# Kernel tuning notes

Hardware: AMD Instinct MI355X
Metric: run time of the kernel (lower is better)

The kernel has to match this reference:

```python
import jax, jax.numpy as jnp
import numpy as np

N_NODES = 50000
N_EDGES = 1600000
IN_CH = 128
OUT_CH = 128
MAX_NORM = 1.0


def setup_inputs() -> dict:
    key = jax.random.key(0)
    k1, k2, k3, k4 = jax.random.split(key, 4)
    x = jax.random.normal(k1, (N_NODES, IN_CH), dtype=jnp.float32)
    edge_index = jax.random.randint(k2, (2, N_EDGES), 0, N_NODES, dtype=jnp.int64)
    # GCNConv lin: weight [out, in] (kaiming-ish init), bias [out] zeros-ish
    W = jax.random.normal(k3, (OUT_CH, IN_CH), dtype=jnp.float32) * (1.0 / np.sqrt(IN_CH))
    b = jax.random.normal(k4, (OUT_CH,), dtype=jnp.float32) * 0.01
    return {"x": x, "edge_index": edge_index, "W": W, "b": b}


def _renorm_cols(W, max_norm):
    # torch.renorm(W, p=2, dim=1, maxnorm): each slice along dim 1 (column of [out,in])
    # is rescaled so its L2 norm <= max_norm.
    norms = jnp.sqrt(jnp.sum(W * W, axis=0, keepdims=True))  # [1, in]
    scale = jnp.where(norms > max_norm, max_norm / norms, 1.0)
    return W * scale


def reference(x, edge_index, W, b):
    N = x.shape[0]
    Wn = _renorm_cols(W, MAX_NORM)
    # Linear transform first (as PyG GCNConv does): h = x @ W^T
    h = jnp.einsum('ni,oi->no', x, Wn)  # [N, out]

    # Add self loops
    row = jnp.concatenate([edge_index[0], jnp.arange(N, dtype=edge_index.dtype)])
    col = jnp.concatenate([edge_index[1], jnp.arange(N, dtype=edge_index.dtype)])

    # Symmetric normalization: deg over destination (col), edge weights = 1
    ones = jnp.ones(row.shape[0], dtype=h.dtype)
    deg = jax.ops.segment_sum(ones, col, num_segments=N)
    deg_inv_sqrt = jnp.where(deg > 0, jax.lax.rsqrt(deg), 0.0)
    norm = deg_inv_sqrt[row] * deg_inv_sqrt[col]  # [E+N]

    # Gather source features, scale, scatter-add to destinations
    msgs = h[row] * norm[:, None]  # [E+N, out]
    out = jax.ops.segment_sum(msgs, col, num_segments=N)
    return out + b
```

## Files before the change

kernel.cpp:

```cpp
#include <hip/hip_runtime.h>

#define N_NODES 50000
#define N_EDGES 1600000
#define CH 128
#define NB 196
#define CHUNK_E 2048
#define NCHUNK 782
#define CAP 12288

#define WS_CURSOR  0
#define WS_ROWPTR  1024
#define WS_DINV    201728
#define WS_SCL     401728
#define WS_SRC     601728
#define WS_Q8      7001728
#define WS_BINS    13401728

typedef __bf16 bf16x8 __attribute__((ext_vector_type(8)));
typedef float f32x4 __attribute__((ext_vector_type(4)));

__device__ __forceinline__ unsigned int pack_bf16(float a, float b) {
    unsigned int ua = __builtin_bit_cast(unsigned int, a);
    unsigned int ub = __builtin_bit_cast(unsigned int, b);
    ua = (ua + 0x7FFFu + ((ua >> 16) & 1u)) >> 16;
    ub = (ub + 0x7FFFu + ((ub >> 16) & 1u)) >> 16;
    return ua | (ub << 16);
}

__global__ __launch_bounds__(256) void k_binA(const int* __restrict__ eidx,
                                              int* __restrict__ cursor,
                                              unsigned int* __restrict__ bins) {
    __shared__ int lc[256];
    __shared__ int lbase[256];
    __shared__ unsigned int stash[CHUNK_E];
    __shared__ int s_st;
    int t = threadIdx.x, c = blockIdx.x;
    lc[t] = 0;
    if (t < 64) {
        int v = eidx[2 * t + 1];
        unsigned long long m = __ballot(v == 0);
        if (t == 0) s_st = (m == ~0ull) ? 2 : 1;
    }
    __syncthreads();
    int st = s_st;
    long base = (long)c * CHUNK_E;
    #pragma unroll
    for (int i = 0; i < CHUNK_E / 256; ++i) {
        long e = base + i * 256 + t;
        unsigned int u = 0xFFFFFFFFu;
        if (e < N_EDGES) {
            int row = eidx[(size_t)st * (size_t)e];
            int col = eidx[(size_t)st * (size_t)(N_EDGES + e)];
            u = (unsigned int)row | ((unsigned int)col << 16);
            atomicAdd(&lc[col >> 8], 1);
        }
        stash[i * 256 + t] = u;
    }
    __syncthreads();
    if (t < NB && lc[t] > 0) lbase[t] = atomicAdd(&cursor[t], lc[t]);
    __syncthreads();
    #pragma unroll
    for (int i = 0; i < CHUNK_E / 256; ++i) {
        unsigned int u = stash[i * 256 + t];
        if (u != 0xFFFFFFFFu) {
            int bb = u >> 24;
            int pos = atomicAdd(&lbase[bb], 1);
            bins[(size_t)bb * CAP + pos] = (u & 0xFFFFu) | (((u >> 16) & 0xFFu) << 16);
        }
    }
}

__global__ __launch_bounds__(256) void k_sort(const unsigned int* __restrict__ bins,
                                              const int* __restrict__ cursor,
                                              int* __restrict__ rowptr,
                                              float* __restrict__ dinv,
                                              int* __restrict__ src) {
    __shared__ int shA[256], shB[256], shC[256];
    __shared__ int s_g0, s_sz;
    int t = threadIdx.x, b = blockIdx.x;
    int v = (t < NB) ? cursor[t] : 0;
    shC[t] = v;
    __syncthreads();
    for (int off = 1; off < 256; off <<= 1) {
        int u = (t >= off) ? shC[t - off] : 0;
        __syncthreads();
        shC[t] += u;
        __syncthreads();
    }
    if (t == b) { s_g0 = shC[t] - v; s_sz = v; }
    __syncthreads();
    int g0 = s_g0, sz = s_sz;
    const unsigned int* reg = bins + (size_t)b * CAP;
    shA[t] = 0;
    __syncthreads();
    for (int i = t; i < sz; i += 256) {
        unsigned int p = reg[i];
        atomicAdd(&shA[(p >> 16) & 255], 1);
    }
    __syncthreads();
    int d = shA[t];
    shC[t] = d;
    __syncthreads();
    for (int off = 1; off < 256; off <<= 1) {
        int u = (t >= off) ? shC[t - off] : 0;
        __syncthreads();
        shC[t] += u;
        __syncthreads();
    }
    int local_rp = g0 + shC[t] - d;
    int n = (b << 8) + t;
    if (n < N_NODES) {
        rowptr[n] = local_rp;
        dinv[n] = rsqrtf((float)(d + 1));
    }
    if (b == NB - 1 && t == 0) rowptr[N_NODES] = N_EDGES;
    shB[t] = local_rp;
    __syncthreads();
    for (int i = t; i < sz; i += 256) {
        unsigned int p = reg[i];
        int pos = atomicAdd(&shB[(p >> 16) & 255], 1);
        src[pos] = (int)(p & 0xFFFFu);
    }
}

__global__ __launch_bounds__(256) void k_gemm(const float* __restrict__ x,
                                              const float* __restrict__ W,
                                              const float* __restrict__ dinv,
                                              unsigned int* __restrict__ q8,
                                              float* __restrict__ scl) {
    __shared__ uint4 SMEM[3072];
    __shared__ float s_scale[128];
    __shared__ float s_part[256];
    uint4* xs = SMEM;
    uint4* wsl = SMEM + 1024;
    float* scratch = (float*)SMEM;
    int t = threadIdx.x;
    int base = blockIdx.x * 64;
    {
        int ct = t & 127, oh = (t >> 7) * 64;
        float s = 0.f;
        #pragma unroll 8
        for (int o = 0; o < 64; ++o) {
            float w = W[(size_t)(oh + o) * CH + ct];
            s += w * w;
        }
        s_part[t] = s;
        __syncthreads();
        if (t < 128) {
            float tot = s_part[t] + s_part[t + 128];
            s_scale[t] = (tot > 1.0f) ? rsqrtf(tot) : 1.0f;
        }
    }
    #pragma unroll
    for (int it = 0; it < 4; ++it) {
        int idx = it * 256 + t;
        int r = idx >> 4, c16 = idx & 15;
        int n = base + r;
        float4 v0 = make_float4(0.f, 0.f, 0.f, 0.f), v1 = v0;
        if (n < N_NODES) {
            v0 = *(const float4*)&x[(size_t)n * CH + c16 * 8];
            v1 = *(const float4*)&x[(size_t)n * CH + c16 * 8 + 4];
        }
        uint4 p;
        p.x = pack_bf16(v0.x, v0.y); p.y = pack_bf16(v0.z, v0.w);
        p.z = pack_bf16(v1.x, v1.y); p.w = pack_bf16(v1.z, v1.w);
        xs[r * 16 + (c16 ^ (r & 7))] = p;
    }
    __syncthreads();
    #pragma unroll
    for (int it = 0; it < 8; ++it) {
        int idx = it * 256 + t;
        int o = idx >> 4, c16 = idx & 15;
        float4 v0 = *(const float4*)&W[(size_t)o * CH + c16 * 8];
        float4 v1 = *(const float4*)&W[(size_t)o * CH + c16 * 8 + 4];
        int k0 = c16 * 8;
        v0.x *= s_scale[k0];     v0.y *= s_scale[k0 + 1];
        v0.z *= s_scale[k0 + 2]; v0.w *= s_scale[k0 + 3];
        v1.x *= s_scale[k0 + 4]; v1.y *= s_scale[k0 + 5];
        v1.z *= s_scale[k0 + 6]; v1.w *= s_scale[k0 + 7];
        uint4 p;
        p.x = pack_bf16(v0.x, v0.y); p.y = pack_bf16(v0.z, v0.w);
        p.z = pack_bf16(v1.x, v1.y); p.w = pack_bf16(v1.z, v1.w);
        wsl[o * 16 + (c16 ^ (o & 7))] = p;
    }
    __syncthreads();
    int w = t >> 6, l = t & 63;
    int lrow = w * 16 + (l & 15);
    int hi = l >> 4;
    bf16x8 a[4];
    #pragma unroll
    for (int ks = 0; ks < 4; ++ks) {
        int c16 = ks * 4 + hi;
        a[ks] = __builtin_bit_cast(bf16x8, xs[lrow * 16 + (c16 ^ (lrow & 7))]);
    }
    float di[4];
    #pragma unroll
    for (int r = 0; r < 4; ++r) {
        int n = base + w * 16 + hi * 4 + r;
        di[r] = (n < N_NODES) ? dinv[n] : 0.f;
    }
    float vals[8][4];
    #pragma unroll
    for (int tc = 0; tc < 8; ++tc) {
        int col = tc * 16 + (l & 15);
        f32x4 acc = {0.f, 0.f, 0.f, 0.f};
        #pragma unroll
        for (int ks = 0; ks < 4; ++ks) {
            int c16 = ks * 4 + hi;
            bf16x8 bf = __builtin_bit_cast(bf16x8, wsl[col * 16 + (c16 ^ (col & 7))]);
            acc = __builtin_amdgcn_mfma_f32_16x16x32_bf16(a[ks], bf, acc, 0, 0, 0);
        }
        #pragma unroll
        for (int r = 0; r < 4; ++r) vals[tc][r] = acc[r] * di[r];
    }
    __syncthreads();
    #pragma unroll
    for (int tc = 0; tc < 8; ++tc) {
        int col = tc * 16 + (l & 15);
        #pragma unroll
        for (int r = 0; r < 4; ++r) {
            int rl = w * 16 + hi * 4 + r;
            scratch[rl * 132 + col] = vals[tc][r];
        }
    }
    __syncthreads();
    int rl = t >> 2, q = t & 3;
    const float4* rp = (const float4*)&scratch[rl * 132 + q * 32];
    float4 f[8];
    float m = 0.f;
    #pragma unroll
    for (int k = 0; k < 8; ++k) {
        f[k] = rp[k];
        m = fmaxf(m, fmaxf(fmaxf(fabsf(f[k].x), fabsf(f[k].y)),
                           fmaxf(fabsf(f[k].z), fabsf(f[k].w))));
    }
    m = fmaxf(m, __shfl_xor(m, 1));
    m = fmaxf(m, __shfl_xor(m, 2));
    float sc = m * (1.0f / 127.0f);
    float inv = (m > 0.f) ? (127.0f / m) : 0.f;
    int n = base + rl;
    if (n < N_NODES) {
        unsigned int u[8];
        #pragma unroll
        for (int k = 0; k < 8; ++k) {
            int b0 = __float2int_rn(f[k].x * inv) + 128;
            int b1 = __float2int_rn(f[k].y * inv) + 128;
            int b2 = __float2int_rn(f[k].z * inv) + 128;
            int b3 = __float2int_rn(f[k].w * inv) + 128;
            u[k] = (unsigned int)b0 | ((unsigned int)b1 << 8) |
                   ((unsigned int)b2 << 16) | ((unsigned int)b3 << 24);
        }
        uint4* qp = (uint4*)&q8[(size_t)n * 32 + q * 8];
        qp[0] = make_uint4(u[0], u[1], u[2], u[3]);
        qp[1] = make_uint4(u[4], u[5], u[6], u[7]);
        if (q == 0) scl[n] = sc;
    }
}

__global__ __launch_bounds__(256) void k_gather(const int* __restrict__ rowptr,
                                                const int* __restrict__ src,
                                                const unsigned int* __restrict__ q8,
                                                const float* __restrict__ scl,
                                                const float* __restrict__ dinv,
                                                const float* __restrict__ b,
                                                float* __restrict__ out) {
    int t = threadIdx.x;
    int wid = t >> 6, lane = t & 63;
    int half = lane >> 5, lc = lane & 31;
    int n = blockIdx.x * 4 + wid;
    if (n >= N_NODES) return;
    int j0 = rowptr[n], j1 = rowptr[n + 1];
    float a0 = 0.f, a1 = 0.f, a2 = 0.f, a3 = 0.f, asum = 0.f;
    int jj = j0;
    for (; jj + 16 <= j1; jj += 16) {
        int rs[8];
        #pragma unroll
        for (int k = 0; k < 8; ++k) rs[k] = src[jj + 2 * k + half];
        float ss[8];
        unsigned int vs[8];
        #pragma unroll
        for (int k = 0; k < 8; ++k) {
            ss[k] = scl[rs[k]];
            vs[k] = q8[((unsigned)rs[k] << 5) + lc];
        }
        #pragma unroll
        for (int k = 0; k < 8; ++k) {
            a0 = fmaf((float)(vs[k] & 0xFFu), ss[k], a0);
            a1 = fmaf((float)((vs[k] >> 8) & 0xFFu), ss[k], a1);
            a2 = fmaf((float)((vs[k] >> 16) & 0xFFu), ss[k], a2);
            a3 = fmaf((float)(vs[k] >> 24), ss[k], a3);
            asum += ss[k];
        }
    }
    for (; jj + 2 <= j1; jj += 2) {
        int r = src[jj + half];
        float sc = scl[r];
        unsigned int v = q8[((unsigned)r << 5) + lc];
        a0 = fmaf((float)(v & 0xFFu), sc, a0);
        a1 = fmaf((float)((v >> 8) & 0xFFu), sc, a1);
        a2 = fmaf((float)((v >> 16) & 0xFFu), sc, a2);
        a3 = fmaf((float)(v >> 24), sc, a3);
        asum += sc;
    }
    if (jj < j1 && half == 0) {
        int r = src[jj];
        float sc = scl[r];
        unsigned int v = q8[((unsigned)r << 5) + lc];
        a0 = fmaf((float)(v & 0xFFu), sc, a0);
        a1 = fmaf((float)((v >> 8) & 0xFFu), sc, a1);
        a2 = fmaf((float)((v >> 16) & 0xFFu), sc, a2);
        a3 = fmaf((float)(v >> 24), sc, a3);
        asum += sc;
    }
    a0 += __shfl_xor(a0, 32);
    a1 += __shfl_xor(a1, 32);
    a2 += __shfl_xor(a2, 32);
    a3 += __shfl_xor(a3, 32);
    asum += __shfl_xor(asum, 32);
    if (half == 0) {
        float di = dinv[n];
        float sc = scl[n];
        unsigned int v = q8[((unsigned)n << 5) + lc];
        float4 bv = *(const float4*)&b[4 * lc];
        float bias128 = 128.0f * asum;
        float s0 = (float)(v & 0xFFu) - 128.0f;
        float s1 = (float)((v >> 8) & 0xFFu) - 128.0f;
        float s2 = (float)((v >> 16) & 0xFFu) - 128.0f;
        float s3 = (float)(v >> 24) - 128.0f;
        float4 o;
        o.x = (a0 - bias128 + s0 * sc) * di + bv.x;
        o.y = (a1 - bias128 + s1 * sc) * di + bv.y;
        o.z = (a2 - bias128 + s2 * sc) * di + bv.z;
        o.w = (a3 - bias128 + s3 * sc) * di + bv.w;
        *(float4*)&out[(size_t)n * CH + 4 * lc] = o;
    }
}

extern "C" void kernel_launch(void* const* d_in, const int* in_sizes, int n_in,
                              void* d_out, int out_size, void* d_ws, size_t ws_size,
                              hipStream_t stream) {
    const float* x = (const float*)d_in[0];
    const int* eidx = (const int*)d_in[1];
    const float* W = (const float*)d_in[2];
    const float* b = (const float*)d_in[3];
    float* out = (float*)d_out;

    char* ws = (char*)d_ws;
    int*   cursor        = (int*)(ws + WS_CURSOR);
    int*   rowptr        = (int*)(ws + WS_ROWPTR);
    float* dinv          = (float*)(ws + WS_DINV);
    float* sclp          = (float*)(ws + WS_SCL);
    int*   srcarr        = (int*)(ws + WS_SRC);
    unsigned int* q8     = (unsigned int*)(ws + WS_Q8);
    unsigned int* bins   = (unsigned int*)(ws + WS_BINS);

    hipMemsetAsync(cursor, 0, NB * sizeof(int), stream);
    k_binA<<<NCHUNK, 256, 0, stream>>>(eidx, cursor, bins);
    k_sort<<<NB, 256, 0, stream>>>(bins, cursor, rowptr, dinv, srcarr);
    k_gemm<<<(N_NODES + 63) / 64, 256, 0, stream>>>(x, W, dinv, q8, sclp);
    k_gather<<<(N_NODES + 3) / 4, 256, 0, stream>>>(rowptr, srcarr, q8, sclp, dinv, b, out);
}
```

Before: 119.0 us.

## Fuse edge binning with GEMM and defer dinv scaling to sort kernel

Edge binning and the quantizing GEMM now run as one launch. The first blocks bin edges and the remaining blocks do the GEMM, so the two independent stages overlap and one launch is removed. Because the GEMM no longer has dinv available, the per-row dinv factor is folded into the per-row quant scale inside the sort kernel (scl *= dinv), which is exact since the scale is per row. Edge loads are vectorized to two edges per thread, and the gather inner loop is unrolled to 32 edges with an 8-edge tail. The cost is more register pressure in the gather and one extra read-modify-write of scl.

Measured after the change: 116.2 us. 1.02x faster.

```diff
diff --git a/kernel.cpp b/kernel.cpp
--- a/kernel.cpp
+++ b/kernel.cpp
@@ -6,6 +6,7 @@
 #define NB 196
 #define CHUNK_E 2048
 #define NCHUNK 782
+#define GEMMB 782
 #define CAP 12288
 
 #define WS_CURSOR  0
@@ -27,115 +28,75 @@
     return ua | (ub << 16);
 }
 
-__global__ __launch_bounds__(256) void k_binA(const int* __restrict__ eidx,
-                                              int* __restrict__ cursor,
-                                              unsigned int* __restrict__ bins) {
-    __shared__ int lc[256];
-    __shared__ int lbase[256];
-    __shared__ unsigned int stash[CHUNK_E];
-    __shared__ int s_st;
-    int t = threadIdx.x, c = blockIdx.x;
-    lc[t] = 0;
-    if (t < 64) {
-        int v = eidx[2 * t + 1];
-        unsigned long long m = __ballot(v == 0);
-        if (t == 0) s_st = (m == ~0ull) ? 2 : 1;
-    }
-    __syncthreads();
-    int st = s_st;
-    long base = (long)c * CHUNK_E;
-    #pragma unroll
-    for (int i = 0; i < CHUNK_E / 256; ++i) {
-        long e = base + i * 256 + t;
-        unsigned int u = 0xFFFFFFFFu;
-        if (e < N_EDGES) {
-            int row = eidx[(size_t)st * (size_t)e];
-            int col = eidx[(size_t)st * (size_t)(N_EDGES + e)];
-            u = (unsigned int)row | ((unsigned int)col << 16);
-            atomicAdd(&lc[col >> 8], 1);
-        }
-        stash[i * 256 + t] = u;
-    }
-    __syncthreads();
-    if (t < NB && lc[t] > 0) lbase[t] = atomicAdd(&cursor[t], lc[t]);
-    __syncthreads();
-    #pragma unroll
-    for (int i = 0; i < CHUNK_E / 256; ++i) {
-        unsigned int u = stash[i * 256 + t];
-        if (u != 0xFFFFFFFFu) {
-            int bb = u >> 24;
-            int pos = atomicAdd(&lbase[bb], 1);
-            bins[(size_t)bb * CAP + pos] = (u & 0xFFFFu) | (((u >> 16) & 0xFFu) << 16);
-        }
-    }
-}
-
-__global__ __launch_bounds__(256) void k_sort(const unsigned int* __restrict__ bins,
-                                              const int* __restrict__ cursor,
-                                              int* __restrict__ rowptr,
-                                              float* __restrict__ dinv,
-                                              int* __restrict__ src) {
-    __shared__ int shA[256], shB[256], shC[256];
-    __shared__ int s_g0, s_sz;
-    int t = threadIdx.x, b = blockIdx.x;
-    int v = (t < NB) ? cursor[t] : 0;
-    shC[t] = v;
-    __syncthreads();
-    for (int off = 1; off < 256; off <<= 1) {
-        int u = (t >= off) ? shC[t - off] : 0;
-        __syncthreads();
-        shC[t] += u;
-        __syncthreads();
-    }
-    if (t == b) { s_g0 = shC[t] - v; s_sz = v; }
-    __syncthreads();
-    int g0 = s_g0, sz = s_sz;
-    const unsigned int* reg = bins + (size_t)b * CAP;
-    shA[t] = 0;
-    __syncthreads();
-    for (int i = t; i < sz; i += 256) {
-        unsigned int p = reg[i];
-        atomicAdd(&shA[(p >> 16) & 255], 1);
-    }
-    __syncthreads();
-    int d = shA[t];
-    shC[t] = d;
-    __syncthreads();
-    for (int off = 1; off < 256; off <<= 1) {
-        int u = (t >= off) ? shC[t - off] : 0;
-        __syncthreads();
-        shC[t] += u;
-        __syncthreads();
-    }
-    int local_rp = g0 + shC[t] - d;
-    int n = (b << 8) + t;
-    if (n < N_NODES) {
-        rowptr[n] = local_rp;
-        dinv[n] = rsqrtf((float)(d + 1));
-    }
-    if (b == NB - 1 && t == 0) rowptr[N_NODES] = N_EDGES;
-    shB[t] = local_rp;
-    __syncthreads();
-    for (int i = t; i < sz; i += 256) {
-        unsigned int p = reg[i];
-        int pos = atomicAdd(&shB[(p >> 16) & 255], 1);
-        src[pos] = (int)(p & 0xFFFFu);
-    }
-}
-
-__global__ __launch_bounds__(256) void k_gemm(const float* __restrict__ x,
-                                              const float* __restrict__ W,
-                                              const float* __restrict__ dinv,
-                                              unsigned int* __restrict__ q8,
-                                              float* __restrict__ scl) {
+__global__ __launch_bounds__(256) void k_fused(const float* __restrict__ x,
+                                               const float* __restrict__ W,
+                                               const int* __restrict__ eidx,
+                                               int* __restrict__ cursor,
+                                               unsigned int* __restrict__ bins,
+                                               unsigned int* __restrict__ q8,
+                                               float* __restrict__ scl) {
     __shared__ uint4 SMEM[3072];
     __shared__ float s_scale[128];
     __shared__ float s_part[256];
+    __shared__ int s_st;
+    int t = threadIdx.x;
+
+    if (blockIdx.x < NCHUNK) {
+        int c = blockIdx.x;
+        int* lc    = (int*)SMEM;
+        int* lbase = (int*)SMEM + 256;
+        unsigned int* stash = (unsigned int*)SMEM + 512;
+        lc[t] = 0;
+        if (t < 64) {
+            int v = eidx[2 * t + 1];
+            unsigned long long m = __ballot(v == 0);
+            if (t == 0) s_st = (m == ~0ull) ? 2 : 1;
+        }
+        __syncthreads();
+        int st = s_st;
+        long base = (long)c * CHUNK_E;
+        #pragma unroll
+        for (int i = 0; i < 4; ++i) {
+            long e0 = base + (long)(i * 256 + t) * 2;
+            unsigned int u0 = 0xFFFFFFFFu, u1 = 0xFFFFFFFFu;
+            if (e0 < N_EDGES) {
+                unsigned int r0, r1, c0, c1;
+                if (st == 2) {
+                    uint4 rw = *(const uint4*)&eidx[2 * e0];
+                    uint4 cw = *(const uint4*)&eidx[2 * (N_EDGES + e0)];
+                    r0 = rw.x; r1 = rw.z; c0 = cw.x; c1 = cw.z;
+                } else {
+                    uint2 rw = *(const uint2*)&eidx[e0];
+                    uint2 cw = *(const uint2*)&eidx[N_EDGES + e0];
+                    r0 = rw.x; r1 = rw.y; c0 = cw.x; c1 = cw.y;
+                }
+                u0 = r0 | (c0 << 16);
+                u1 = r1 | (c1 << 16);
+                atomicAdd(&lc[c0 >> 8], 1);
+                atomicAdd(&lc[c1 >> 8], 1);
+            }
+            stash[i * 512 + 2 * t]     = u0;
+            stash[i * 512 + 2 * t + 1] = u1;
+        }
+        __syncthreads();
+        if (t < NB && lc[t] > 0) lbase[t] = atomicAdd(&cursor[t], lc[t]);
+        __syncthreads();
+        #pragma unroll
+        for (int i = 0; i < 8; ++i) {
+            unsigned int u = stash[i * 256 + t];
+            if (u != 0xFFFFFFFFu) {
+                int bb = u >> 24;
+                int pos = atomicAdd(&lbase[bb], 1);
+                bins[(size_t)bb * CAP + pos] = (u & 0xFFFFu) | (((u >> 16) & 0xFFu) << 16);
+            }
+        }
+        return;
+    }
+
     uint4* xs = SMEM;
     uint4* wsl = SMEM + 1024;
     float* scratch = (float*)SMEM;
-    int t = threadIdx.x;
-    int base = blockIdx.x * 64;
+    int base = (blockIdx.x - NCHUNK) * 64;
     {
         int ct = t & 127, oh = (t >> 7) * 64;
         float s = 0.f;
@@ -193,12 +154,6 @@
         int c16 = ks * 4 + hi;
         a[ks] = __builtin_bit_cast(bf16x8, xs[lrow * 16 + (c16 ^ (lrow & 7))]);
     }
-    float di[4];
-    #pragma unroll
-    for (int r = 0; r < 4; ++r) {
-        int n = base + w * 16 + hi * 4 + r;
-        di[r] = (n < N_NODES) ? dinv[n] : 0.f;
-    }
     float vals[8][4];
     #pragma unroll
     for (int tc = 0; tc < 8; ++tc) {
@@ -211,7 +166,7 @@
             acc = __builtin_amdgcn_mfma_f32_16x16x32_bf16(a[ks], bf, acc, 0, 0, 0);
         }
         #pragma unroll
-        for (int r = 0; r < 4; ++r) vals[tc][r] = acc[r] * di[r];
+        for (int r = 0; r < 4; ++r) vals[tc][r] = acc[r];
     }
     __syncthreads();
     #pragma unroll
@@ -254,6 +209,62 @@
         qp[0] = make_uint4(u[0], u[1], u[2], u[3]);
         qp[1] = make_uint4(u[4], u[5], u[6], u[7]);
         if (q == 0) scl[n] = sc;
+    }
+}
+
+__global__ __launch_bounds__(256) void k_sort(const unsigned int* __restrict__ bins,
+                                              const int* __restrict__ cursor,
+                                              int* __restrict__ rowptr,
+                                              float* __restrict__ dinv,
+                                              float* __restrict__ scl,
+                                              int* __restrict__ src) {
+    __shared__ int shA[256], shB[256], shC[256];
+    __shared__ int s_g0, s_sz;
+    int t = threadIdx.x, b = blockIdx.x;
+    int v = (t < NB) ? cursor[t] : 0;
+    shC[t] = v;
+    __syncthreads();
+    for (int off = 1; off < 256; off <<= 1) {
+        int u = (t >= off) ? shC[t - off] : 0;
+        __syncthreads();
+        shC[t] += u;
+        __syncthreads();
+    }
+    if (t == b) { s_g0 = shC[t] - v; s_sz = v; }
+    __syncthreads();
+    int g0 = s_g0, sz = s_sz;
+    const unsigned int* reg = bins + (size_t)b * CAP;
+    shA[t] = 0;
+    __syncthreads();
+    for (int i = t; i < sz; i += 256) {
+        unsigned int p = reg[i];
+        atomicAdd(&shA[(p >> 16) & 255], 1);
+    }
+    __syncthreads();
+    int d = shA[t];
+    shC[t] = d;
+    __syncthreads();
+    for (int off = 1; off < 256; off <<= 1) {
+        int u = (t >= off) ? shC[t - off] : 0;
+        __syncthreads();
+        shC[t] += u;
+        __syncthreads();
+    }
+    int local_rp = g0 + shC[t] - d;
+    int n = (b << 8) + t;
+    if (n < N_NODES) {
+        rowptr[n] = local_rp;
+        float dv = rsqrtf((float)(d + 1));
+        dinv[n] = dv;
+        scl[n] *= dv;
+    }
+    if (b == NB - 1 && t == 0) rowptr[N_NODES] = N_EDGES;
+    shB[t] = local_rp;
+    __syncthreads();
+    for (int i = t; i < sz; i += 256) {
+        unsigned int p = reg[i];
+        int pos = atomicAdd(&shB[(p >> 16) & 255], 1);
+        src[pos] = (int)(p & 0xFFFFu);
     }
 }
 
@@ -272,24 +283,39 @@
     int j0 = rowptr[n], j1 = rowptr[n + 1];
     float a0 = 0.f, a1 = 0.f, a2 = 0.f, a3 = 0.f, asum = 0.f;
     int jj = j0;
-    for (; jj + 16 <= j1; jj += 16) {
-        int rs[8];
-        #pragma unroll
-        for (int k = 0; k < 8; ++k) rs[k] = src[jj + 2 * k + half];
-        float ss[8];
-        unsigned int vs[8];
-        #pragma unroll
-        for (int k = 0; k < 8; ++k) {
+    for (; jj + 32 <= j1; jj += 32) {
+        int rs[16];
+        #pragma unroll
+        for (int k = 0; k < 16; ++k) rs[k] = src[jj + 2 * k + half];
+        float ss[16];
+        unsigned int vs[16];
+        #pragma unroll
+        for (int k = 0; k < 16; ++k) {
             ss[k] = scl[rs[k]];
             vs[k] = q8[((unsigned)rs[k] << 5) + lc];
         }
         #pragma unroll
-        for (int k = 0; k < 8; ++k) {
+        for (int k = 0; k < 16; ++k) {
             a0 = fmaf((float)(vs[k] & 0xFFu), ss[k], a0);
             a1 = fmaf((float)((vs[k] >> 8) & 0xFFu), ss[k], a1);
             a2 = fmaf((float)((vs[k] >> 16) & 0xFFu), ss[k], a2);
             a3 = fmaf((float)(vs[k] >> 24), ss[k], a3);
             asum += ss[k];
+        }
+    }
+    for (; jj + 8 <= j1; jj += 8) {
+        int rs[4];
+        #pragma unroll
+        for (int k = 0; k < 4; ++k) rs[k] = src[jj + 2 * k + half];
+        #pragma unroll
+        for (int k = 0; k < 4; ++k) {
+            float sc = scl[rs[k]];
+            unsigned int v = q8[((unsigned)rs[k] << 5) + lc];
+            a0 = fmaf((float)(v & 0xFFu), sc, a0);
+            a1 = fmaf((float)((v >> 8) & 0xFFu), sc, a1);
+            a2 = fmaf((float)((v >> 16) & 0xFFu), sc, a2);
+            a3 = fmaf((float)(v >> 24), sc, a3);
+            asum += sc;
         }
     }
     for (; jj + 2 <= j1; jj += 2) {
@@ -355,8 +381,7 @@
     unsigned int* bins   = (unsigned int*)(ws + WS_BINS);
 
     hipMemsetAsync(cursor, 0, NB * sizeof(int), stream);
-    k_binA<<<NCHUNK, 256, 0, stream>>>(eidx, cursor, bins);
-    k_sort<<<NB, 256, 0, stream>>>(bins, cursor, rowptr, dinv, srcarr);
-    k_gemm<<<(N_NODES + 63) / 64, 256, 0, stream>>>(x, W, dinv, q8, sclp);
+    k_fused<<<NCHUNK + GEMMB, 256, 0, stream>>>(x, W, eidx, cursor, bins, q8, sclp);
+    k_sort<<<NB, 256, 0, stream>>>(bins, cursor, rowptr, dinv, sclp, srcarr);
     k_gather<<<(N_NODES + 3) / 4, 256, 0, stream>>>(rowptr, srcarr, q8, sclp, dinv, b, out);
 }
```
